# Optimization experiments

Measured on AMD Instinct MI355X. Metric: run time of the kernel, lower is better.

## Reference

```python
import jax, jax.numpy as jnp
import numpy as np

N, C, T, H, W = 8, 512, 8, 32, 32
CI = 256          # inter_channels = in_channels // 2
CA = 128          # audio feature dim (hard-coded nn.Linear(128, in_channels))
BN_EPS = 1e-5
LN_EPS = 1e-5


def setup_inputs() -> dict:
    key = jax.random.key(0)
    ks = jax.random.split(key, 8)
    s = 0.02
    f32 = jnp.float32
    return {
        "x": jax.random.normal(ks[0], (N, C, T, H, W), f32),
        "audio": jax.random.normal(ks[1], (N, T, CA), f32),
        "align_W": jax.random.normal(ks[2], (C, CA), f32) * s,
        "align_b": jnp.zeros((C,), f32),
        "Wg": jax.random.normal(ks[3], (CI, C), f32) * s,
        "bg": jnp.zeros((CI,), f32),
        "Wth": jax.random.normal(ks[4], (CI, C), f32) * s,
        "bth": jnp.zeros((CI,), f32),
        "Wph": jax.random.normal(ks[5], (CI, C), f32) * s,
        "bph": jnp.zeros((CI,), f32),
        "Wz": jax.random.normal(ks[6], (C, CI), f32) * s,
        "bz": jnp.zeros((C,), f32),
        "bn_gamma": jnp.ones((C,), f32),
        "bn_beta": jnp.zeros((C,), f32),
        "ln_gamma": jnp.ones((C,), f32),
        "ln_beta": jnp.zeros((C,), f32),
    }


def reference(x, audio, align_W, align_b, Wg, bg, Wth, bth, Wph, bph,
              Wz, bz, bn_gamma, bn_beta, ln_gamma, ln_beta):
    n, c, t, h, w = x.shape
    thw = t * h * w

    # align_channel: Linear(128, C) + ReLU on audio (N,T,128) -> (N,T,C)
    audio_temp = jax.nn.relu(jnp.einsum('ntk,ck->ntc', audio, align_W) + align_b)
    a = audio_temp.transpose(0, 2, 1)  # (N,C,T); broadcast over (H,W) kept implicit

    # 1x1x1 conv projections (== per-token linear maps)
    g_x = (jnp.einsum('oc,ncthw->nthwo', Wg, x) + bg).reshape(n, thw, CI)      # (N,THW,CI)
    theta_x = (jnp.einsum('oc,ncthw->nthwo', Wth, x) + bth).reshape(n, thw, CI)
    phi_a = jnp.einsum('oc,nct->not', Wph, a) + bph[None, :, None]             # (N,CI,T)

    # mode='dot' attention. phi(audio) is constant over (h,w): the full score
    # matrix f[n,s,(t,h,w)] equals f_small[n,s,t], so f@g factorizes exactly.
    f_small = jnp.einsum('nsi,nit->nst', theta_x, phi_a)   # (N,THW,T)
    f_div = f_small / thw                                  # f / N_tokens
    G = g_x.reshape(n, t, h * w, CI).sum(axis=2)           # (N,T,CI): sum of g over repeated hw
    y = jnp.einsum('nst,nto->nso', f_div, G)               # (N,THW,CI)
    y = y.transpose(0, 2, 1).reshape(n, CI, t, h, w)

    # W_z: 1x1x1 conv (CI->C) + BatchNorm3d (training-mode batch stats)
    W_y = jnp.einsum('oc,ncthw->nothw', Wz, y) + bz[None, :, None, None, None]
    mu = W_y.mean(axis=(0, 2, 3, 4), keepdims=True)
    var = W_y.var(axis=(0, 2, 3, 4), keepdims=True)
    W_y = (W_y - mu) * jax.lax.rsqrt(var + BN_EPS)
    W_y = W_y * bn_gamma[None, :, None, None, None] + bn_beta[None, :, None, None, None]

    # residual blend + LayerNorm over channel dim
    z = 0.5 * W_y + 0.5 * x
    zp = z.transpose(0, 2, 3, 4, 1)  # (N,T,H,W,C)
    mu2 = zp.mean(axis=-1, keepdims=True)
    var2 = zp.var(axis=-1, keepdims=True)
    zp = (zp - mu2) * jax.lax.rsqrt(var2 + LN_EPS) * ln_gamma + ln_beta
    z = zp.transpose(0, 4, 1, 2, 3)  # (N,C,T,H,W)
    return z, audio_temp
```

## Files before the change

### kernel.cpp

```cpp
#include <hip/hip_runtime.h>


typedef float __attribute__((ext_vector_type(2))) f32x2;

__global__ __launch_bounds__(256) void k_xsum(const float* __restrict__ x, float* __restrict__ xs)
{
    int row = blockIdx.x * 4 + (threadIdx.x >> 6);
    int lane = threadIdx.x & 63;
    const float4* p = reinterpret_cast<const float4*>(x + (size_t)row * 1024);
    float s = 0.f;
    #pragma unroll
    for (int k = 0; k < 4; ++k) {
        float4 v = p[lane + 64 * k];
        s += v.x + v.y + v.z + v.w;
    }
    for (int off = 32; off > 0; off >>= 1) s += __shfl_down(s, off);
    if (lane == 0) xs[row] = s;
}

__global__ __launch_bounds__(256) void k_pre(
    const float* __restrict__ audio, const float* __restrict__ alignW, const float* __restrict__ alignB,
    const float* __restrict__ Wph, const float* __restrict__ bph,
    const float* __restrict__ Wth, const float* __restrict__ bth,
    const float* __restrict__ xs, const float* __restrict__ Wg, const float* __restrict__ bg,
    const float* __restrict__ Wz,
    float* __restrict__ outA, float* __restrict__ constT, float* __restrict__ M,
    float* __restrict__ GW)
{
    int b = blockIdx.x; int n = b >> 3; int t = b & 7; int tid = threadIdx.x;
    __shared__ float al[128];
    __shared__ float atl[512];
    __shared__ float phil[256];
    __shared__ float red[256];
    __shared__ float xsl[512];
    __shared__ float gl[256];
    if (tid < 128) al[tid] = audio[(n * 8 + t) * 128 + tid];
    __syncthreads();
    for (int c = tid; c < 512; c += 256) {
        float a0 = alignB[c], a1 = 0.f, a2 = 0.f, a3 = 0.f;
        const float* Wr = alignW + c * 128;
        #pragma unroll 4
        for (int k = 0; k < 128; k += 4) {
            a0 += al[k] * Wr[k];         a1 += al[k + 1] * Wr[k + 1];
            a2 += al[k + 2] * Wr[k + 2]; a3 += al[k + 3] * Wr[k + 3];
        }
        float acc = fmaxf((a0 + a1) + (a2 + a3), 0.f);
        atl[c] = acc;
        outA[(n * 8 + t) * 512 + c] = acc;
    }
    __syncthreads();
    {
        int i = tid;
        float a0 = bph[i], a1 = 0.f, a2 = 0.f, a3 = 0.f;
        const float* Wr = Wph + i * 512;
        #pragma unroll 4
        for (int c = 0; c < 512; c += 4) {
            a0 += Wr[c] * atl[c];         a1 += Wr[c + 1] * atl[c + 1];
            a2 += Wr[c + 2] * atl[c + 2]; a3 += Wr[c + 3] * atl[c + 3];
        }
        float acc = (a0 + a1) + (a2 + a3);
        phil[i] = acc;
        red[i] = acc * bth[i];
    }
    __syncthreads();
    for (int sr = 128; sr > 0; sr >>= 1) {
        if (tid < sr) red[tid] += red[tid + sr];
        __syncthreads();
    }
    if (tid == 0) constT[n * 8 + t] = red[0];
    for (int c = tid; c < 512; c += 256) {
        float a0 = 0.f, a1 = 0.f, a2 = 0.f, a3 = 0.f;
        #pragma unroll 4
        for (int i = 0; i < 256; i += 4) {
            a0 += Wth[i * 512 + c] * phil[i];
            a1 += Wth[(i + 1) * 512 + c] * phil[i + 1];
            a2 += Wth[(i + 2) * 512 + c] * phil[i + 2];
            a3 += Wth[(i + 3) * 512 + c] * phil[i + 3];
        }
        M[n * 4096 + c * 8 + t] = (a0 + a1) + (a2 + a3);
    }
    for (int c = tid; c < 512; c += 256) xsl[c] = xs[(n * 512 + c) * 8 + t];
    __syncthreads();
    {
        int o = tid;
        float a0 = 1024.f * bg[o], a1 = 0.f, a2 = 0.f, a3 = 0.f;
        const float* Wr = Wg + o * 512;
        #pragma unroll 4
        for (int c = 0; c < 512; c += 4) {
            a0 += Wr[c] * xsl[c];         a1 += Wr[c + 1] * xsl[c + 1];
            a2 += Wr[c + 2] * xsl[c + 2]; a3 += Wr[c + 3] * xsl[c + 3];
        }
        gl[o] = (a0 + a1) + (a2 + a3);
    }
    __syncthreads();
    for (int c = tid; c < 512; c += 256) {
        float a0 = 0.f, a1 = 0.f, a2 = 0.f, a3 = 0.f;
        const float* Wr = Wz + c * 256;
        #pragma unroll 4
        for (int o = 0; o < 256; o += 4) {
            a0 += Wr[o] * gl[o];         a1 += Wr[o + 1] * gl[o + 1];
            a2 += Wr[o + 2] * gl[o + 2]; a3 += Wr[o + 3] * gl[o + 3];
        }
        GW[(n * 8 + t) * 512 + c] = (a0 + a1) + (a2 + a3);
    }
}

__global__ __launch_bounds__(512, 4) void k_fsmall(
    const float* __restrict__ x, const float* __restrict__ M,
    const float* __restrict__ constT, float* __restrict__ fs,
    float* __restrict__ Part)
{
    int b = blockIdx.x; int n = b >> 6; int s0 = (b & 63) << 7;
    int tid = threadIdx.x; int lane = tid & 63; int wv = tid >> 6;
    __shared__ float Ml[512][8];
    {
        const float4* src = reinterpret_cast<const float4*>(M + n * 4096);
        float4* dst = reinterpret_cast<float4*>(&Ml[0][0]);
        for (int i = tid; i < 1024; i += 512) dst[i] = src[i];
    }
    __syncthreads();
    const float* xb = x + (size_t)n * 4194304 + s0 + lane * 2;
    float2 p2[8];
    #pragma unroll
    for (int k = 0; k < 8; ++k) p2[k] = make_float2(0.f, 0.f);
    #pragma unroll 16
    for (int j = 0; j < 64; ++j) {
        int c = wv * 64 + j;
        float2 xv = *reinterpret_cast<const float2*>(xb + (size_t)c * 8192);
        float4 m0 = *reinterpret_cast<const float4*>(&Ml[c][0]);
        float4 m1 = *reinterpret_cast<const float4*>(&Ml[c][4]);
        p2[0].x = fmaf(xv.x, m0.x, p2[0].x); p2[0].y = fmaf(xv.y, m0.x, p2[0].y);
        p2[1].x = fmaf(xv.x, m0.y, p2[1].x); p2[1].y = fmaf(xv.y, m0.y, p2[1].y);
        p2[2].x = fmaf(xv.x, m0.z, p2[2].x); p2[2].y = fmaf(xv.y, m0.z, p2[2].y);
        p2[3].x = fmaf(xv.x, m0.w, p2[3].x); p2[3].y = fmaf(xv.y, m0.w, p2[3].y);
        p2[4].x = fmaf(xv.x, m1.x, p2[4].x); p2[4].y = fmaf(xv.y, m1.x, p2[4].y);
        p2[5].x = fmaf(xv.x, m1.y, p2[5].x); p2[5].y = fmaf(xv.y, m1.y, p2[5].y);
        p2[6].x = fmaf(xv.x, m1.z, p2[6].x); p2[6].y = fmaf(xv.y, m1.z, p2[6].y);
        p2[7].x = fmaf(xv.x, m1.w, p2[7].x); p2[7].y = fmaf(xv.y, m1.w, p2[7].y);
    }
    __shared__ float ldsT[8][8][130];
    #pragma unroll
    for (int k = 0; k < 8; ++k)
        *reinterpret_cast<float2*>(&ldsT[wv][k][lane * 2]) = p2[k];
    __syncthreads();
    __shared__ float partm[2][44];
    if (tid < 128) {
        int tok = tid; int wq = tid >> 6;
        const float* ct = constT + n * 8;
        float q[8];
        #pragma unroll
        for (int k = 0; k < 8; ++k) {
            float v = ct[k];
            #pragma unroll
            for (int g = 0; g < 8; ++g) v += ldsT[g][k][tok];
            q[k] = v;
        }
        float4* op = reinterpret_cast<float4*>(fs + ((size_t)n * 8192 + s0 + tok) * 8);
        op[0] = make_float4(q[0], q[1], q[2], q[3]);
        op[1] = make_float4(q[4], q[5], q[6], q[7]);
        float mom[44];
        {
            int idx = 8;
            for (int t1 = 0; t1 < 8; ++t1) {
                mom[t1] = q[t1];
                for (int t2 = t1; t2 < 8; ++t2) { mom[idx] = q[t1] * q[t2]; ++idx; }
            }
        }
        for (int k = 0; k < 44; ++k)
            for (int off = 32; off > 0; off >>= 1) mom[k] += __shfl_down(mom[k], off);
        if ((tid & 63) == 0)
            for (int k = 0; k < 44; ++k) partm[wq][k] = mom[k];
    }
    __syncthreads();
    if (tid < 44) Part[b * 44 + tid] = partm[0][tid] + partm[1][tid];
}

__global__ __launch_bounds__(512, 4) void k_final(
    const float* __restrict__ x, const float* __restrict__ fs,
    const float* __restrict__ Part, const float* __restrict__ GW,
    const float* __restrict__ bz, const float* __restrict__ bng, const float* __restrict__ bnb,
    const float* __restrict__ lng, const float* __restrict__ lnb,
    float* __restrict__ outZ)
{
    int b = blockIdx.x; int n = b >> 6; int s0 = (b & 63) << 7;
    int tid = threadIdx.x; int lane = tid & 63; int wv = tid >> 6;
    __shared__ float GWl[512][8];
    __shared__ float4 PKl[512];
    __shared__ float redS[2][8][130];
    __shared__ float Fl[64];
    __shared__ float S2l[512];
    if (tid < 352) {
        int n2 = tid / 44, k = tid % 44;
        float v = 0.f;
        for (int i = 0; i < 64; ++i) v += Part[(n2 * 64 + i) * 44 + k];
        if (k < 8) Fl[n2 * 8 + k] = v;
        else {
            int kk = k - 8; int t1 = 0;
            while (kk >= 8 - t1) { kk -= 8 - t1; ++t1; }
            int t2 = t1 + kk;
            S2l[n2 * 64 + t1 * 8 + t2] = v;
            S2l[n2 * 64 + t2 * 8 + t1] = v;
        }
    }
    __syncthreads();
    {
        int c = tid;
        const float r = 1.f / 8192.f;
        float meanu = 0.f, e2 = 0.f;
        float gmine[8];
        for (int n2 = 0; n2 < 8; ++n2) {
            float g[8];
            #pragma unroll
            for (int t = 0; t < 8; ++t) g[t] = GW[(n2 * 8 + t) * 512 + c];
            if (n2 == n) {
                #pragma unroll
                for (int t = 0; t < 8; ++t) gmine[t] = g[t];
            }
            #pragma unroll
            for (int t = 0; t < 8; ++t) meanu += Fl[n2 * 8 + t] * g[t];
            for (int t1 = 0; t1 < 8; ++t1)
                #pragma unroll
                for (int t2 = 0; t2 < 8; ++t2) e2 += S2l[n2 * 64 + t1 * 8 + t2] * g[t1] * g[t2];
        }
        const float invCnt = 1.f / 65536.f;
        meanu *= r * invCnt;
        e2 *= r * r * invCnt;
        float var = fmaxf(e2 - meanu * meanu, 0.f);
        float bzv = bz[c];
        float sc = bng[c] * rsqrtf(var + 1e-5f);
        float sh = bnb[c] - (meanu + bzv) * sc;
        float4 pk;
        pk.x = 0.5f * (bzv * sc + sh);
        pk.y = lng[c];
        pk.z = lnb[c];
        pk.w = 0.f;
        PKl[c] = pk;
        float scale = 0.5f * r * sc;
        #pragma unroll
        for (int t = 0; t < 8; ++t) GWl[c][t] = gmine[t] * scale;
    }
    __syncthreads();
    float4 fA0, fB0, fA1, fB1;
    {
        const float4* fp = reinterpret_cast<const float4*>(fs + ((size_t)n * 8192 + s0 + lane * 2) * 8);
        fA0 = fp[0]; fB0 = fp[1]; fA1 = fp[2]; fB1 = fp[3];
    }
    const size_t xbase = (size_t)n * 4194304 + s0 + lane * 2;
    float2 s1 = make_float2(0.f, 0.f), sq = make_float2(0.f, 0.f);
    #pragma unroll 16
    for (int j = 0; j < 64; ++j) {
        int c = wv * 64 + j;
        float2 xv = *reinterpret_cast<const float2*>(&x[xbase + (size_t)c * 8192]);
        float4 g0 = *reinterpret_cast<const float4*>(&GWl[c][0]);
        float4 g1 = *reinterpret_cast<const float4*>(&GWl[c][4]);
        float pk0 = PKl[c].x;
        float z0 = pk0 + 0.5f * xv.x
            + fA0.x * g0.x + fA0.y * g0.y + fA0.z * g0.z + fA0.w * g0.w
            + fB0.x * g1.x + fB0.y * g1.y + fB0.z * g1.z + fB0.w * g1.w;
        float z1 = pk0 + 0.5f * xv.y
            + fA1.x * g0.x + fA1.y * g0.y + fA1.z * g0.z + fA1.w * g0.w
            + fB1.x * g1.x + fB1.y * g1.y + fB1.z * g1.z + fB1.w * g1.w;
        s1.x += z0; sq.x += z0 * z0;
        s1.y += z1; sq.y += z1 * z1;
    }
    *reinterpret_cast<float2*>(&redS[0][wv][lane * 2]) = s1;
    *reinterpret_cast<float2*>(&redS[1][wv][lane * 2]) = sq;
    __syncthreads();
    float mean0, rstd0, mean1, rstd1;
    {
        int t0 = lane * 2, t1 = lane * 2 + 1;
        float a0 = 0.f, q0 = 0.f, a1 = 0.f, q1 = 0.f;
        #pragma unroll
        for (int g = 0; g < 8; ++g) {
            a0 += redS[0][g][t0]; q0 += redS[1][g][t0];
            a1 += redS[0][g][t1]; q1 += redS[1][g][t1];
        }
        mean0 = a0 * (1.f / 512.f);
        rstd0 = rsqrtf(fmaxf(q0 * (1.f / 512.f) - mean0 * mean0, 0.f) + 1e-5f);
        mean1 = a1 * (1.f / 512.f);
        rstd1 = rsqrtf(fmaxf(q1 * (1.f / 512.f) - mean1 * mean1, 0.f) + 1e-5f);
    }
    #pragma unroll 16
    for (int j = 0; j < 64; ++j) {
        int c = wv * 64 + j;
        float2 xv = *reinterpret_cast<const float2*>(&x[xbase + (size_t)c * 8192]);
        float4 g0 = *reinterpret_cast<const float4*>(&GWl[c][0]);
        float4 g1 = *reinterpret_cast<const float4*>(&GWl[c][4]);
        float4 pk = PKl[c];
        float z0 = pk.x + 0.5f * xv.x
            + fA0.x * g0.x + fA0.y * g0.y + fA0.z * g0.z + fA0.w * g0.w
            + fB0.x * g1.x + fB0.y * g1.y + fB0.z * g1.z + fB0.w * g1.w;
        float z1 = pk.x + 0.5f * xv.y
            + fA1.x * g0.x + fA1.y * g0.y + fA1.z * g0.z + fA1.w * g0.w
            + fB1.x * g1.x + fB1.y * g1.y + fB1.z * g1.z + fB1.w * g1.w;
        f32x2 o;
        o.x = (z0 - mean0) * rstd0 * pk.y + pk.z;
        o.y = (z1 - mean1) * rstd1 * pk.y + pk.z;
        __builtin_nontemporal_store(o, reinterpret_cast<f32x2*>(&outZ[xbase + (size_t)c * 8192]));
    }
}

extern "C" void kernel_launch(void* const* d_in, const int* in_sizes, int n_in,
                              void* d_out, int out_size, void* d_ws, size_t ws_size,
                              hipStream_t stream)
{
    const float* x      = (const float*)d_in[0];
    const float* audio  = (const float*)d_in[1];
    const float* alignW = (const float*)d_in[2];
    const float* alignB = (const float*)d_in[3];
    const float* Wg     = (const float*)d_in[4];
    const float* bg     = (const float*)d_in[5];
    const float* Wth    = (const float*)d_in[6];
    const float* bth    = (const float*)d_in[7];
    const float* Wph    = (const float*)d_in[8];
    const float* bph    = (const float*)d_in[9];
    const float* Wz     = (const float*)d_in[10];
    const float* bz     = (const float*)d_in[11];
    const float* bng    = (const float*)d_in[12];
    const float* bnb    = (const float*)d_in[13];
    const float* lng    = (const float*)d_in[14];
    const float* lnb    = (const float*)d_in[15];
    float* outZ = (float*)d_out;
    float* outA = outZ + 33554432;

    uintptr_t pa = ((uintptr_t)d_ws + 255) & ~(uintptr_t)255;
    float* w = (float*)pa;

    float* constT = w;
    float* M      = w + 64;
    float* XS     = w + 32832;
    float* GW     = w + 65600;
    float* Part   = w + 98368;
    float* fsm    = w + 120896;

    k_xsum<<<8192, 256, 0, stream>>>(x, XS);
    k_pre<<<64, 256, 0, stream>>>(audio, alignW, alignB, Wph, bph, Wth, bth,
                                  XS, Wg, bg, Wz, outA, constT, M, GW);
    k_fsmall<<<512, 512, 0, stream>>>(x, M, constT, fsm, Part);
    k_final<<<512, 512, 0, stream>>>(x, fsm, Part, GW, bz, bng, bnb, lng, lnb, outZ);
}
```

Measured before the change: 181.4 us.

## Merge xsum with audio prelude and move Wg/Wz projection into fsmall launch

Folds the x-row-sum kernel into the same launch as the audio/phi/M precompute, using extra blocks, so the two independent jobs run concurrently. The Wg/Wz projection that depended on xsum moves into the fsmall launch as 64 extra blocks, which takes it off the serial chain before fsmall. The inner products are rewritten with float4 loads and multiple accumulators, and xsum output is stored transposed for contiguous reads. This removes one launch and the serialization between stages, at the cost of heterogeneous blocks and the larger shared-memory footprint applied to every stage2 block.

```diff
diff --git a/kernel.cpp b/kernel.cpp
--- a/kernel.cpp
+++ b/kernel.cpp
@@ -3,64 +3,76 @@
 
 typedef float __attribute__((ext_vector_type(2))) f32x2;
 
-__global__ __launch_bounds__(256) void k_xsum(const float* __restrict__ x, float* __restrict__ xs)
-{
-    int row = blockIdx.x * 4 + (threadIdx.x >> 6);
-    int lane = threadIdx.x & 63;
-    const float4* p = reinterpret_cast<const float4*>(x + (size_t)row * 1024);
-    float s = 0.f;
-    #pragma unroll
-    for (int k = 0; k < 4; ++k) {
-        float4 v = p[lane + 64 * k];
-        s += v.x + v.y + v.z + v.w;
-    }
-    for (int off = 32; off > 0; off >>= 1) s += __shfl_down(s, off);
-    if (lane == 0) xs[row] = s;
-}
-
-__global__ __launch_bounds__(256) void k_pre(
-    const float* __restrict__ audio, const float* __restrict__ alignW, const float* __restrict__ alignB,
+__device__ __forceinline__ float hsum4(float4 v) { return (v.x + v.y) + (v.z + v.w); }
+__device__ __forceinline__ void fma4v(float4& a, float4 w, float4 x) {
+    a.x = fmaf(w.x, x.x, a.x); a.y = fmaf(w.y, x.y, a.y);
+    a.z = fmaf(w.z, x.z, a.z); a.w = fmaf(w.w, x.w, a.w);
+}
+
+__global__ __launch_bounds__(256) void k_stage1(
+    const float* __restrict__ x, const float* __restrict__ audio,
+    const float* __restrict__ alignW, const float* __restrict__ alignB,
     const float* __restrict__ Wph, const float* __restrict__ bph,
     const float* __restrict__ Wth, const float* __restrict__ bth,
-    const float* __restrict__ xs, const float* __restrict__ Wg, const float* __restrict__ bg,
-    const float* __restrict__ Wz,
     float* __restrict__ outA, float* __restrict__ constT, float* __restrict__ M,
-    float* __restrict__ GW)
+    float* __restrict__ xsT)
 {
-    int b = blockIdx.x; int n = b >> 3; int t = b & 7; int tid = threadIdx.x;
+    int b = blockIdx.x; int tid = threadIdx.x;
     __shared__ float al[128];
     __shared__ float atl[512];
     __shared__ float phil[256];
     __shared__ float red[256];
-    __shared__ float xsl[512];
-    __shared__ float gl[256];
-    if (tid < 128) al[tid] = audio[(n * 8 + t) * 128 + tid];
-    __syncthreads();
-    for (int c = tid; c < 512; c += 256) {
-        float a0 = alignB[c], a1 = 0.f, a2 = 0.f, a3 = 0.f;
-        const float* Wr = alignW + c * 128;
+    if (b >= 64) {
+        int row = (b - 64) * 4 + (tid >> 6);
+        int lane = tid & 63;
+        const float4* p = reinterpret_cast<const float4*>(x + (size_t)row * 1024);
+        float s = 0.f;
+        #pragma unroll
+        for (int k = 0; k < 4; ++k) {
+            float4 v = p[lane + 64 * k];
+            s += v.x + v.y + v.z + v.w;
+        }
+        for (int off = 32; off > 0; off >>= 1) s += __shfl_down(s, off);
+        if (lane == 0) {
+            int n = row >> 12, c = (row >> 3) & 511, t = row & 7;
+            xsT[((size_t)n * 8 + t) * 512 + c] = s;
+        }
+        return;
+    }
+    int n = b >> 3; int t = b & 7;
+    if (tid < 32)
+        reinterpret_cast<float4*>(al)[tid] =
+            reinterpret_cast<const float4*>(audio + (n * 8 + t) * 128)[tid];
+    __syncthreads();
+    {
+        const float4* W0 = reinterpret_cast<const float4*>(alignW + (size_t)tid * 128);
+        const float4* W1 = reinterpret_cast<const float4*>(alignW + (size_t)(tid + 256) * 128);
+        const float4* A4 = reinterpret_cast<const float4*>(al);
+        float4 s00 = {0,0,0,0}, s01 = {0,0,0,0}, s10 = {0,0,0,0}, s11 = {0,0,0,0};
+        #pragma unroll
+        for (int k = 0; k < 32; k += 2) {
+            float4 a0 = A4[k], a1 = A4[k + 1];
+            fma4v(s00, W0[k], a0); fma4v(s01, W0[k + 1], a1);
+            fma4v(s10, W1[k], a0); fma4v(s11, W1[k + 1], a1);
+        }
+        float v0 = fmaxf(alignB[tid] + hsum4(s00) + hsum4(s01), 0.f);
+        float v1 = fmaxf(alignB[tid + 256] + hsum4(s10) + hsum4(s11), 0.f);
+        atl[tid] = v0;       outA[(n * 8 + t) * 512 + tid] = v0;
+        atl[tid + 256] = v1; outA[(n * 8 + t) * 512 + tid + 256] = v1;
+    }
+    __syncthreads();
+    {
+        const float4* Wp = reinterpret_cast<const float4*>(Wph + (size_t)tid * 512);
+        const float4* At = reinterpret_cast<const float4*>(atl);
+        float4 s0 = {0,0,0,0}, s1 = {0,0,0,0}, s2 = {0,0,0,0}, s3 = {0,0,0,0};
         #pragma unroll 4
         for (int k = 0; k < 128; k += 4) {
-            a0 += al[k] * Wr[k];         a1 += al[k + 1] * Wr[k + 1];
-            a2 += al[k + 2] * Wr[k + 2]; a3 += al[k + 3] * Wr[k + 3];
-        }
-        float acc = fmaxf((a0 + a1) + (a2 + a3), 0.f);
-        atl[c] = acc;
-        outA[(n * 8 + t) * 512 + c] = acc;
-    }
-    __syncthreads();
-    {
-        int i = tid;
-        float a0 = bph[i], a1 = 0.f, a2 = 0.f, a3 = 0.f;
-        const float* Wr = Wph + i * 512;
-        #pragma unroll 4
-        for (int c = 0; c < 512; c += 4) {
-            a0 += Wr[c] * atl[c];         a1 += Wr[c + 1] * atl[c + 1];
-            a2 += Wr[c + 2] * atl[c + 2]; a3 += Wr[c + 3] * atl[c + 3];
-        }
-        float acc = (a0 + a1) + (a2 + a3);
-        phil[i] = acc;
-        red[i] = acc * bth[i];
+            fma4v(s0, Wp[k], At[k]);         fma4v(s1, Wp[k + 1], At[k + 1]);
+            fma4v(s2, Wp[k + 2], At[k + 2]); fma4v(s3, Wp[k + 3], At[k + 3]);
+        }
+        float acc = bph[tid] + (hsum4(s0) + hsum4(s1)) + (hsum4(s2) + hsum4(s3));
+        phil[tid] = acc;
+        red[tid] = acc * bth[tid];
     }
     __syncthreads();
     for (int sr = 128; sr > 0; sr >>= 1) {
@@ -68,58 +80,75 @@
         __syncthreads();
     }
     if (tid == 0) constT[n * 8 + t] = red[0];
-    for (int c = tid; c < 512; c += 256) {
-        float a0 = 0.f, a1 = 0.f, a2 = 0.f, a3 = 0.f;
-        #pragma unroll 4
+    {
+        float a0 = 0, a1 = 0, a2 = 0, a3 = 0, c0 = 0, c1 = 0, c2 = 0, c3 = 0;
+        #pragma unroll 2
         for (int i = 0; i < 256; i += 4) {
-            a0 += Wth[i * 512 + c] * phil[i];
-            a1 += Wth[(i + 1) * 512 + c] * phil[i + 1];
-            a2 += Wth[(i + 2) * 512 + c] * phil[i + 2];
-            a3 += Wth[(i + 3) * 512 + c] * phil[i + 3];
-        }
-        M[n * 4096 + c * 8 + t] = (a0 + a1) + (a2 + a3);
-    }
-    for (int c = tid; c < 512; c += 256) xsl[c] = xs[(n * 512 + c) * 8 + t];
-    __syncthreads();
-    {
-        int o = tid;
-        float a0 = 1024.f * bg[o], a1 = 0.f, a2 = 0.f, a3 = 0.f;
-        const float* Wr = Wg + o * 512;
-        #pragma unroll 4
-        for (int c = 0; c < 512; c += 4) {
-            a0 += Wr[c] * xsl[c];         a1 += Wr[c + 1] * xsl[c + 1];
-            a2 += Wr[c + 2] * xsl[c + 2]; a3 += Wr[c + 3] * xsl[c + 3];
-        }
-        gl[o] = (a0 + a1) + (a2 + a3);
-    }
-    __syncthreads();
-    for (int c = tid; c < 512; c += 256) {
-        float a0 = 0.f, a1 = 0.f, a2 = 0.f, a3 = 0.f;
-        const float* Wr = Wz + c * 256;
-        #pragma unroll 4
-        for (int o = 0; o < 256; o += 4) {
-            a0 += Wr[o] * gl[o];         a1 += Wr[o + 1] * gl[o + 1];
-            a2 += Wr[o + 2] * gl[o + 2]; a3 += Wr[o + 3] * gl[o + 3];
-        }
-        GW[(n * 8 + t) * 512 + c] = (a0 + a1) + (a2 + a3);
-    }
-}
-
-__global__ __launch_bounds__(512, 4) void k_fsmall(
+            float p0 = phil[i], p1 = phil[i + 1], p2 = phil[i + 2], p3 = phil[i + 3];
+            const float* W = Wth + (size_t)i * 512 + tid;
+            a0 = fmaf(W[0], p0, a0);    a1 = fmaf(W[512], p1, a1);
+            a2 = fmaf(W[1024], p2, a2); a3 = fmaf(W[1536], p3, a3);
+            const float* W2 = W + 256;
+            c0 = fmaf(W2[0], p0, c0);    c1 = fmaf(W2[512], p1, c1);
+            c2 = fmaf(W2[1024], p2, c2); c3 = fmaf(W2[1536], p3, c3);
+        }
+        M[n * 4096 + tid * 8 + t] = (a0 + a1) + (a2 + a3);
+        M[n * 4096 + (tid + 256) * 8 + t] = (c0 + c1) + (c2 + c3);
+    }
+}
+
+__global__ __launch_bounds__(512, 4) void k_stage2(
     const float* __restrict__ x, const float* __restrict__ M,
-    const float* __restrict__ constT, float* __restrict__ fs,
-    float* __restrict__ Part)
+    const float* __restrict__ constT, const float* __restrict__ xsT,
+    const float* __restrict__ Wg, const float* __restrict__ bg,
+    const float* __restrict__ Wz,
+    float* __restrict__ fs, float* __restrict__ Part, float* __restrict__ GW)
 {
-    int b = blockIdx.x; int n = b >> 6; int s0 = (b & 63) << 7;
-    int tid = threadIdx.x; int lane = tid & 63; int wv = tid >> 6;
+    int b = blockIdx.x; int tid = threadIdx.x;
     __shared__ float Ml[512][8];
+    __shared__ float ldsT[8][8][130];
+    __shared__ float partm[2][44];
+    __shared__ float xsl[512];
+    __shared__ float gl[256];
+    if (b >= 512) {
+        int b2 = b - 512; int n = b2 >> 3; int t = b2 & 7;
+        xsl[tid] = xsT[((size_t)n * 8 + t) * 512 + tid];
+        __syncthreads();
+        if (tid < 256) {
+            const float4* Wr = reinterpret_cast<const float4*>(Wg + (size_t)tid * 512);
+            const float4* X4 = reinterpret_cast<const float4*>(xsl);
+            float4 s0 = {0,0,0,0}, s1 = {0,0,0,0}, s2 = {0,0,0,0}, s3 = {0,0,0,0};
+            #pragma unroll 4
+            for (int k = 0; k < 128; k += 4) {
+                fma4v(s0, Wr[k], X4[k]);         fma4v(s1, Wr[k + 1], X4[k + 1]);
+                fma4v(s2, Wr[k + 2], X4[k + 2]); fma4v(s3, Wr[k + 3], X4[k + 3]);
+            }
+            gl[tid] = 1024.f * bg[tid] + (hsum4(s0) + hsum4(s1)) + (hsum4(s2) + hsum4(s3));
+        }
+        __syncthreads();
+        {
+            const float4* Wr = reinterpret_cast<const float4*>(Wz + (size_t)tid * 256);
+            const float4* G4 = reinterpret_cast<const float4*>(gl);
+            float4 s0 = {0,0,0,0}, s1 = {0,0,0,0}, s2 = {0,0,0,0}, s3 = {0,0,0,0};
+            #pragma unroll 4
+            for (int k = 0; k < 64; k += 4) {
+                fma4v(s0, Wr[k], G4[k]);         fma4v(s1, Wr[k + 1], G4[k + 1]);
+                fma4v(s2, Wr[k + 2], G4[k + 2]); fma4v(s3, Wr[k + 3], G4[k + 3]);
+            }
+            GW[((size_t)n * 8 + t) * 512 + tid] =
+                (hsum4(s0) + hsum4(s1)) + (hsum4(s2) + hsum4(s3));
+        }
+        return;
+    }
+    int n = b >> 6; int s0i = (b & 63) << 7;
+    int lane = tid & 63; int wv = tid >> 6;
     {
         const float4* src = reinterpret_cast<const float4*>(M + n * 4096);
         float4* dst = reinterpret_cast<float4*>(&Ml[0][0]);
         for (int i = tid; i < 1024; i += 512) dst[i] = src[i];
     }
     __syncthreads();
-    const float* xb = x + (size_t)n * 4194304 + s0 + lane * 2;
+    const float* xb = x + (size_t)n * 4194304 + s0i + lane * 2;
     float2 p2[8];
     #pragma unroll
     for (int k = 0; k < 8; ++k) p2[k] = make_float2(0.f, 0.f);
@@ -138,12 +167,10 @@
         p2[6].x = fmaf(xv.x, m1.z, p2[6].x); p2[6].y = fmaf(xv.y, m1.z, p2[6].y);
         p2[7].x = fmaf(xv.x, m1.w, p2[7].x); p2[7].y = fmaf(xv.y, m1.w, p2[7].y);
     }
-    __shared__ float ldsT[8][8][130];
     #pragma unroll
     for (int k = 0; k < 8; ++k)
         *reinterpret_cast<float2*>(&ldsT[wv][k][lane * 2]) = p2[k];
     __syncthreads();
-    __shared__ float partm[2][44];
     if (tid < 128) {
         int tok = tid; int wq = tid >> 6;
         const float* ct = constT + n * 8;
@@ -155,7 +182,7 @@
             for (int g = 0; g < 8; ++g) v += ldsT[g][k][tok];
             q[k] = v;
         }
-        float4* op = reinterpret_cast<float4*>(fs + ((size_t)n * 8192 + s0 + tok) * 8);
+        float4* op = reinterpret_cast<float4*>(fs + ((size_t)n * 8192 + s0i + tok) * 8);
         op[0] = make_float4(q[0], q[1], q[2], q[3]);
         op[1] = make_float4(q[4], q[5], q[6], q[7]);
         float mom[44];
@@ -333,9 +360,8 @@
     float* Part   = w + 98368;
     float* fsm    = w + 120896;
 
-    k_xsum<<<8192, 256, 0, stream>>>(x, XS);
-    k_pre<<<64, 256, 0, stream>>>(audio, alignW, alignB, Wph, bph, Wth, bth,
-                                  XS, Wg, bg, Wz, outA, constT, M, GW);
-    k_fsmall<<<512, 512, 0, stream>>>(x, M, constT, fsm, Part);
+    k_stage1<<<8256, 256, 0, stream>>>(x, audio, alignW, alignB, Wph, bph, Wth, bth,
+                                       outA, constT, M, XS);
+    k_stage2<<<576, 512, 0, stream>>>(x, M, constT, XS, Wg, bg, Wz, fsm, Part, GW);
     k_final<<<512, 512, 0, stream>>>(x, fsm, Part, GW, bz, bng, bnb, lng, lnb, outZ);
 }
```

Measured after the change: 170.5 us, median of 2. 1.06x faster.
